# Optimization experiments

Measured on AMD Instinct MI355X. Metric: run time of the kernel, lower is better.

The kernel has to match this reference:

```python
import jax, jax.numpy as jnp
import numpy as np

B, NEG = 4, 33          # queries, candidates per query
N, R = 10000, 256       # entities, relation types (even; R//2 direct)
D, L = 64, 6            # hidden dim, conv layers
E, ER = 200000, 80000   # entity edges, edges per relation graph (hh/ht/th/tt)
F = 2 * D
EPS = 1e-5


def _ln(x, s, b):
    m = jnp.mean(x, -1, keepdims=True)
    v = jnp.mean((x - m) ** 2, -1, keepdims=True)
    return (x - m) * jax.lax.rsqrt(v + EPS) * s + b


def _conv(x, boundary, relation, src, dst, etype, p):
    # GeneralizedRelationalConv (dependent=False, project_relations=True):
    # distmult message, sum aggregate + boundary self-loop, update=relu(LN(Linear([x,agg])))
    p1w, p1b, p2w, p2b, lw, lb, lns, lnb = p
    rel = jax.nn.relu(relation @ p1w + p1b) @ p2w + p2b     # relation projection MLP
    msg = x[:, src, :] * rel[:, etype, :]                   # [B, Eg, D] gathered messages
    agg = jnp.zeros_like(boundary).at[:, dst, :].add(msg) + boundary
    out = jnp.concatenate([x, agg], -1) @ lw + lb
    return jax.nn.relu(_ln(out, lns, lnb))


def _entity_bf(rel_reps, h0, r0, src, dst, etype, params):
    # NBFNet Bellman-Ford over the entity graph, query-conditioned boundary
    q = rel_reps[jnp.arange(B), r0]                         # [B, D]
    boundary = jnp.zeros((B, N, D), q.dtype).at[jnp.arange(B), h0].add(q)
    x = boundary
    for i in range(L):
        x = _conv(x, boundary, rel_reps, src, dst, etype,
                  tuple(t[i] for t in params)) + x          # short_cut residual
    nq = jnp.broadcast_to(q[:, None, :], (B, N, D))
    return jnp.concatenate([x, nq], -1)                     # [B, N, 2D]


def _forward(floats, ints):
    (e1p1w, e1p1b, e1p2w, e1p2b, e1lw, e1lb, e1lns, e1lnb,
     e2p1w, e2p1b, e2p2w, e2p2b, e2lw, e2lb, e2lns, e2lnb,
     e2m1w, e2m1b, e2m2w, e2m2b,
     rp1w, rp1b, rp2w, rp2b, rlw, rlb, rlns, rlnb, nmw, nmb) = floats
    edge_src, edge_dst, edge_type, rel_src, rel_dst, rel_etype, batch = ints
    h0 = batch[:, 0, 0]
    t_idx = batch[:, :, 1]
    r0 = batch[:, 0, 2]
    e1p = (e1p1w, e1p1b, e1p2w, e1p2b, e1lw, e1lb, e1lns, e1lnb)
    # ---- RelNet over the 4 relation graphs (nodes=relations, edge types=entities) ----
    node_reps = jnp.ones((B, N, D), e1p1w.dtype)
    q = jnp.ones((B, D), e1p1w.dtype)
    boundary = jnp.zeros((B, R, D), q.dtype).at[jnp.arange(B), r0].add(q)
    x = boundary
    for i in range(L):
        h = sum(_conv(x, boundary, node_reps, rel_src[g], rel_dst[g], rel_etype[g],
                      (rp1w[g, i], rp1b[g, i], rp2w[g, i], rp2b[g, i],
                       rlw[g, i], rlb[g, i], rlns[g, i], rlnb[g, i]))
                for g in range(4))
        x = h + x                                           # short_cut
        if i == 0:
            # entity_model_1 refreshes the per-entity (relation-graph edge type) reps
            feat = _entity_bf(x, h0, r0, edge_src, edge_dst, edge_type, e1p)
            node_reps = feat @ nmw + nmb                    # [B, N, D]
    rel_reps = x                                            # [B, R, D]
    # ---- EntityNet 2: score candidates ----
    e2p = (e2p1w, e2p1b, e2p2w, e2p2b, e2lw, e2lb, e2lns, e2lnb)
    feat2 = _entity_bf(rel_reps, h0, r0, edge_src, edge_dst, edge_type, e2p)
    g = jnp.take_along_axis(feat2, jnp.broadcast_to(t_idx[:, :, None], (B, NEG, F)), axis=1)
    score = (jax.nn.relu(g @ e2m1w + e2m1b) @ e2m2w + e2m2b)[..., 0]
    return score                                            # [B, NEG]


def setup_inputs():
    key = jax.random.key(0)
    ks = iter(jax.random.split(key, 64))
    def w(shape, std=0.08):
        return jax.random.normal(next(ks), shape, jnp.float32) * std
    inp = {}
    inp["edge_src"] = jax.random.randint(next(ks), (E,), 0, N, jnp.int32)
    inp["edge_dst"] = jax.random.randint(next(ks), (E,), 0, N, jnp.int32)
    inp["edge_type"] = jax.random.randint(next(ks), (E,), 0, R, jnp.int32)
    inp["rel_src"] = jax.random.randint(next(ks), (4, ER), 0, R, jnp.int32)
    inp["rel_dst"] = jax.random.randint(next(ks), (4, ER), 0, R, jnp.int32)
    inp["rel_etype"] = jax.random.randint(next(ks), (4, ER), 0, N, jnp.int32)
    h = jax.random.randint(next(ks), (B, 1), 0, N, jnp.int32)
    t = jax.random.randint(next(ks), (B, NEG), 0, N, jnp.int32)
    r = jax.random.randint(next(ks), (B, 1), 0, R // 2, jnp.int32)
    inp["batch"] = jnp.stack([jnp.broadcast_to(h, (B, NEG)), t,
                              jnp.broadcast_to(r, (B, NEG))], -1)
    for pre in ("e1", "e2"):
        inp[pre + "p1w"] = w((L, D, D)); inp[pre + "p1b"] = jnp.zeros((L, D))
        inp[pre + "p2w"] = w((L, D, D)); inp[pre + "p2b"] = jnp.zeros((L, D))
        inp[pre + "lw"] = w((L, F, D));  inp[pre + "lb"] = jnp.zeros((L, D))
        inp[pre + "lns"] = jnp.ones((L, D)); inp[pre + "lnb"] = jnp.zeros((L, D))
    inp["e2m1w"] = w((F, F)); inp["e2m1b"] = jnp.zeros((F,))
    inp["e2m2w"] = w((F, 1)); inp["e2m2b"] = jnp.zeros((1,))
    inp["rp1w"] = w((4, L, D, D)); inp["rp1b"] = jnp.zeros((4, L, D))
    inp["rp2w"] = w((4, L, D, D)); inp["rp2b"] = jnp.zeros((4, L, D))
    inp["rlw"] = w((4, L, F, D));  inp["rlb"] = jnp.zeros((4, L, D))
    inp["rlns"] = jnp.ones((4, L, D)); inp["rlnb"] = jnp.zeros((4, L, D))
    inp["nmw"] = w((F, D)); inp["nmb"] = jnp.zeros((D,))
    return inp


def reference(e1p1w, e1p1b, e1p2w, e1p2b, e1lw, e1lb, e1lns, e1lnb,
              e2p1w, e2p1b, e2p2w, e2p2b, e2lw, e2lb, e2lns, e2lnb,
              e2m1w, e2m1b, e2m2w, e2m2b,
              rp1w, rp1b, rp2w, rp2b, rlw, rlb, rlns, rlnb, nmw, nmb,
              edge_src, edge_dst, edge_type, rel_src, rel_dst, rel_etype, batch):
    floats = (e1p1w, e1p1b, e1p2w, e1p2b, e1lw, e1lb, e1lns, e1lnb,
              e2p1w, e2p1b, e2p2w, e2p2b, e2lw, e2lb, e2lns, e2lnb,
              e2m1w, e2m1b, e2m2w, e2m2b,
              rp1w, rp1b, rp2w, rp2b, rlw, rlb, rlns, rlnb, nmw, nmb)
    ints = (edge_src, edge_dst, edge_type, rel_src, rel_dst, rel_etype, batch)
    return _forward(floats, ints)
```

## Files before the change

### kernel.cpp

```cpp
#include <hip/hip_runtime.h>

constexpr int kB   = 4;
constexpr int kNEG = 33;
constexpr int kN   = 10000;
constexpr int kR   = 256;
constexpr int kD   = 64;
constexpr int kL   = 6;
constexpr int kE   = 200000;
constexpr int kER  = 80000;

typedef const float* fp;
typedef __attribute__((ext_vector_type(8))) short bf16x8;
typedef __attribute__((ext_vector_type(4))) float f32x4;

__device__ __forceinline__ float rdlane(float v, int l) {
  return __uint_as_float(__builtin_amdgcn_readlane(__float_as_uint(v), l));
}
__device__ __forceinline__ float wave_sum64(float v) {
  #pragma unroll
  for (int o = 32; o > 0; o >>= 1) v += __shfl_xor(v, o, 64);
  return v;
}
__device__ __forceinline__ float group_sum16(float v) {
  #pragma unroll
  for (int o = 8; o > 0; o >>= 1) v += __shfl_xor(v, o, 64);
  return v;
}
__device__ __forceinline__ short f2bf(float x) {
  unsigned u = __float_as_uint(x);
  unsigned r = (u + 0x7fffu + ((u >> 16) & 1u)) >> 16;
  return (short)r;
}
__device__ __forceinline__ float bf2f_u(unsigned short s) {
  return __uint_as_float(((unsigned)s) << 16);
}
__device__ __forceinline__ float bf2f(short s) { return bf2f_u((unsigned short)s); }

__global__ void k_fill(float* __restrict__ p, float v, int n) {
  int i = blockIdx.x * blockDim.x + threadIdx.x;
  int stride = gridDim.x * blockDim.x;
  for (; i < n; i += stride) p[i] = v;
}
__global__ void k_zero_i(int* __restrict__ p, int n) {
  int i = blockIdx.x * blockDim.x + threadIdx.x;
  int stride = gridDim.x * blockDim.x;
  for (; i < n; i += stride) p[i] = 0;
}
__global__ void k_add_row(float* __restrict__ dst, const int* __restrict__ batch) {
  int tid = threadIdx.x;
  int b = tid >> 6, d = tid & 63;
  int row = batch[b * kNEG * 3 + 2];
  dst[((size_t)b * kR + row) * 64 + d] += 1.0f;
}
__global__ void k_add_row_ent(float* __restrict__ dst, const int* __restrict__ batch,
                              const float* __restrict__ q) {
  int tid = threadIdx.x;
  int b = tid >> 6, d = tid & 63;
  int row = batch[b * kNEG * 3];
  dst[((size_t)b * kN + row) * 64 + d] += q[b * 64 + d];
}
__global__ void k_get_q(float* __restrict__ q, const float* __restrict__ relx,
                        const int* __restrict__ batch) {
  int tid = threadIdx.x;
  int b = tid >> 6, d = tid & 63;
  int r0 = batch[b * kNEG * 3 + 2];
  q[b * 64 + d] = relx[((size_t)b * kR + r0) * 64 + d];
}

__global__ void k_hist(const int* __restrict__ dst, int ne, int* __restrict__ cnt) {
  int i = blockIdx.x * blockDim.x + threadIdx.x;
  if (i < ne) atomicAdd(&cnt[dst[i]], 1);
}
__global__ void k_fill_csr(const int* __restrict__ src, const int* __restrict__ dst,
                           const int* __restrict__ et, int ne,
                           int* __restrict__ cursor, int2* __restrict__ out) {
  int i = blockIdx.x * blockDim.x + threadIdx.x;
  if (i < ne) {
    int p = atomicAdd(&cursor[dst[i]], 1);
    out[p] = make_int2(src[i], et[i]);
  }
}
__global__ void k_hist_rel_lds(const int* __restrict__ rel_dst, int* __restrict__ cnt) {
  int g = blockIdx.y;
  __shared__ int lc[256];
  lc[threadIdx.x] = 0;
  __syncthreads();
  int lo = blockIdx.x * 8000, hi = min(lo + 8000, kER);
  for (int e = lo + threadIdx.x; e < hi; e += 256)
    atomicAdd(&lc[rel_dst[(size_t)g * kER + e]], 1);
  __syncthreads();
  int c = lc[threadIdx.x];
  if (c) atomicAdd(&cnt[g * 256 + threadIdx.x], c);
}
__global__ void k_fill_rel_lds(const int* __restrict__ src, const int* __restrict__ dst,
                               const int* __restrict__ et,
                               int* __restrict__ cursor, int2* __restrict__ out) {
  int g = blockIdx.y;
  __shared__ int lc[256];
  lc[threadIdx.x] = 0;
  __syncthreads();
  int lo = blockIdx.x * 8000, hi = min(lo + 8000, kER);
  const int* db = dst + (size_t)g * kER;
  for (int e = lo + threadIdx.x; e < hi; e += 256)
    atomicAdd(&lc[db[e]], 1);
  __syncthreads();
  int c = lc[threadIdx.x];
  __syncthreads();
  lc[threadIdx.x] = c ? atomicAdd(&cursor[g * 257 + threadIdx.x], c) : 0;
  __syncthreads();
  for (int e = lo + threadIdx.x; e < hi; e += 256) {
    int bin = db[e];
    int p = atomicAdd(&lc[bin], 1);
    out[(size_t)g * kER + p] = make_int2(src[(size_t)g * kER + e], et[(size_t)g * kER + e]);
  }
}
__global__ void k_scan_multi(const int* __restrict__ cnt, int* __restrict__ start,
                             int* __restrict__ cursor, int n, int cstride, int sstride) {
  const int* c = cnt + (size_t)blockIdx.x * cstride;
  int* st = start + (size_t)blockIdx.x * sstride;
  int* cu = cursor + (size_t)blockIdx.x * sstride;
  __shared__ int part[256];
  int t = threadIdx.x;
  int chunk = (n + 255) / 256;
  int lo = t * chunk, hi = min(lo + chunk, n);
  int s = 0;
  for (int i = lo; i < hi; ++i) s += c[i];
  part[t] = s;
  __syncthreads();
  if (t == 0) { int run = 0; for (int i = 0; i < 256; ++i) { int v = part[i]; part[i] = run; run += v; } }
  __syncthreads();
  int run = part[t];
  for (int i = lo; i < hi; ++i) { st[i] = run; cu[i] = run; run += c[i]; }
  if (t == 255) st[n] = run;
}

__global__ void k_packw(const float* __restrict__ w1, const float* __restrict__ w2,
                        short* __restrict__ w1h, short* __restrict__ w1l,
                        short* __restrict__ w2h, short* __restrict__ w2l) {
  int pg = blockIdx.x;
  for (int i = threadIdx.x; i < 4096; i += 256) {
    int t = i & 7, lane = (i >> 3) & 63, nt = (i >> 9) & 3, ks = i >> 11;
    int mr = lane & 15, kg = lane >> 4;
    int src = pg * 4096 + (ks * 32 + kg * 8 + t) * 64 + nt * 16 + mr;
    int dst = pg * 4096 + i;
    float v1 = w1[src]; short h1 = f2bf(v1);
    w1h[dst] = h1; w1l[dst] = f2bf(v1 - bf2f(h1));
    float v2 = w2[src]; short h2 = f2bf(v2);
    w2h[dst] = h2; w2l[dst] = f2bf(v2 - bf2f(h2));
  }
}
__global__ void k_packw_e(const float* __restrict__ w, short* __restrict__ wh, short* __restrict__ wl) {
  int set = blockIdx.x;
  for (int i = threadIdx.x; i < 8192; i += 256) {
    int t = i & 7, lane = (i >> 3) & 63, nt = (i >> 9) & 3, ks = i >> 11;
    int mr = lane & 15, kg = lane >> 4;
    int src = set * 8192 + (ks * 32 + kg * 8 + t) * 64 + nt * 16 + mr;
    int dst = set * 8192 + i;
    float v = w[src]; short h = f2bf(v);
    wh[dst] = h; wl[dst] = f2bf(v - bf2f(h));
  }
}

__global__ void __launch_bounds__(256) k_mlp_mfma(
    const float* __restrict__ in, const short* __restrict__ w1h, const short* __restrict__ w1l,
    const float* __restrict__ b1, const short* __restrict__ w2h, const short* __restrict__ w2l,
    const float* __restrict__ b2, int layer, unsigned short* __restrict__ out) {
  int g = blockIdx.y;
  int pg = g * kL + layer;
  int w = threadIdx.x >> 6, lane = threadIdx.x & 63;
  int mrow = lane & 15, kgrp = lane >> 4;
  int r0 = blockIdx.x * 64 + w * 16;
  __shared__ float hbuf[4][16][68];
  const float* xp = in + (size_t)(r0 + mrow) * 64 + kgrp * 8;
  bf16x8 a1h[2], a1l[2];
  #pragma unroll
  for (int ks = 0; ks < 2; ++ks) {
    #pragma unroll
    for (int t = 0; t < 8; ++t) {
      float v = xp[ks * 32 + t];
      short h = f2bf(v); a1h[ks][t] = h; a1l[ks][t] = f2bf(v - bf2f(h));
    }
  }
  const bf16x8* B1h = (const bf16x8*)(w1h + (size_t)pg * 4096);
  const bf16x8* B1l = (const bf16x8*)(w1l + (size_t)pg * 4096);
  #pragma unroll
  for (int nt = 0; nt < 4; ++nt) {
    f32x4 c = {0.f, 0.f, 0.f, 0.f};
    #pragma unroll
    for (int ks = 0; ks < 2; ++ks) {
      bf16x8 bh = B1h[(ks * 4 + nt) * 64 + lane];
      bf16x8 bl = B1l[(ks * 4 + nt) * 64 + lane];
      c = __builtin_amdgcn_mfma_f32_16x16x32_bf16(a1h[ks], bh, c, 0, 0, 0);
      c = __builtin_amdgcn_mfma_f32_16x16x32_bf16(a1h[ks], bl, c, 0, 0, 0);
      c = __builtin_amdgcn_mfma_f32_16x16x32_bf16(a1l[ks], bh, c, 0, 0, 0);
    }
    int col = nt * 16 + mrow;
    float bv = b1[pg * 64 + col];
    #pragma unroll
    for (int rg = 0; rg < 4; ++rg)
      hbuf[w][kgrp * 4 + rg][col] = fmaxf(c[rg] + bv, 0.f);
  }
  __syncthreads();
  bf16x8 a2h[2], a2l[2];
  #pragma unroll
  for (int ks = 0; ks < 2; ++ks) {
    #pragma unroll
    for (int t = 0; t < 8; ++t) {
      float v = hbuf[w][mrow][ks * 32 + kgrp * 8 + t];
      short h = f2bf(v); a2h[ks][t] = h; a2l[ks][t] = f2bf(v - bf2f(h));
    }
  }
  const bf16x8* B2h = (const bf16x8*)(w2h + (size_t)pg * 4096);
  const bf16x8* B2l = (const bf16x8*)(w2l + (size_t)pg * 4096);
  unsigned short* ob = out + (size_t)g * kB * kN * 64;
  #pragma unroll
  for (int nt = 0; nt < 4; ++nt) {
    f32x4 c = {0.f, 0.f, 0.f, 0.f};
    #pragma unroll
    for (int ks = 0; ks < 2; ++ks) {
      bf16x8 bh = B2h[(ks * 4 + nt) * 64 + lane];
      bf16x8 bl = B2l[(ks * 4 + nt) * 64 + lane];
      c = __builtin_amdgcn_mfma_f32_16x16x32_bf16(a2h[ks], bh, c, 0, 0, 0);
      c = __builtin_amdgcn_mfma_f32_16x16x32_bf16(a2h[ks], bl, c, 0, 0, 0);
      c = __builtin_amdgcn_mfma_f32_16x16x32_bf16(a2l[ks], bh, c, 0, 0, 0);
    }
    int col = nt * 16 + mrow;
    float bv = b2[pg * 64 + col];
    #pragma unroll
    for (int rg = 0; rg < 4; ++rg) {
      int grow = r0 + kgrp * 4 + rg;
      int bb = grow / kN;
      int nn = grow - bb * kN;
      ob[(size_t)nn * 256 + col * 4 + bb] = (unsigned short)f2bf(c[rg] + bv);
    }
  }
}

__global__ void __launch_bounds__(256) k_mlp_rel6(
    const float* __restrict__ in, fp p1w, fp p1b, fp p2w, fp p2b,
    unsigned short* __restrict__ out) {
  int j = blockIdx.y;
  int row = blockIdx.x * 4 + (threadIdx.x >> 6);
  int lane = threadIdx.x & 63;
  fp W1 = p1w + (size_t)j * 4096;
  fp W2 = p2w + (size_t)j * 4096;
  float xv = in[(size_t)row * 64 + lane];
  float a = p1b[j * 64 + lane];
  float wbuf[8];
  #pragma unroll
  for (int kk = 0; kk < 64; kk += 8) {
    #pragma unroll
    for (int u = 0; u < 8; ++u) wbuf[u] = W1[(kk + u) * 64 + lane];
    #pragma unroll
    for (int u = 0; u < 8; ++u) a = fmaf(rdlane(xv, kk + u), wbuf[u], a);
  }
  a = fmaxf(a, 0.f);
  float c = p2b[j * 64 + lane];
  #pragma unroll
  for (int kk = 0; kk < 64; kk += 8) {
    #pragma unroll
    for (int u = 0; u < 8; ++u) wbuf[u] = W2[(kk + u) * 64 + lane];
    #pragma unroll
    for (int u = 0; u < 8; ++u) c = fmaf(rdlane(a, kk + u), wbuf[u], c);
  }
  int b = row >> 8, r = row & 255;
  out[((size_t)j * kR + r) * 256 + lane * 4 + b] = (unsigned short)f2bf(c);
}

__global__ void k_gate0(fp p1w, fp p1b, fp p2w, fp p2b, float* __restrict__ gate0) {
  int g = threadIdx.x >> 6, lane = threadIdx.x & 63;
  int pg = g * kL;
  float a = p1b[pg * 64 + lane];
  #pragma unroll
  for (int k = 0; k < 64; ++k) a += p1w[(size_t)pg * 4096 + k * 64 + lane];
  a = fmaxf(a, 0.f);
  float c = p2b[pg * 64 + lane];
  #pragma unroll
  for (int k = 0; k < 64; ++k)
    c = fmaf(rdlane(a, k), p2w[(size_t)pg * 4096 + k * 64 + lane], c);
  gate0[g * 64 + lane] = c;
}
__global__ void k_rel_agg0(const int* __restrict__ rel_start, const int2* __restrict__ rel_edges,
                           const int* __restrict__ batch, const float* __restrict__ gate0,
                           float* __restrict__ agg) {
  int wid = (blockIdx.x * blockDim.x + threadIdx.x) >> 6;
  int lane = threadIdx.x & 63;
  int g = wid >> 10, rem = wid & 1023, b = rem >> 8, r = rem & 255;
  int r0 = batch[b * kNEG * 3 + 2];
  const int* start = rel_start + g * 257;
  const int2* edges = rel_edges + (size_t)g * kER;
  int s0 = start[r], s1 = start[r + 1];
  int cnt = 0;
  for (int base = s0; base < s1; base += 64) {
    int e = base + lane;
    bool m = false;
    if (e < s1) m = (edges[e].x == r0);
    cnt += (int)__popcll(__ballot(m));
  }
  agg[(size_t)wid * 64 + lane] = gate0[g * 64 + lane] * (float)cnt + ((r == r0) ? 1.f : 0.f);
}

__global__ void __launch_bounds__(256) k_gather_rel_all(
    const float* __restrict__ rxi, const unsigned short* __restrict__ gateN,
    const int* __restrict__ rel_start, const int2* __restrict__ rel_edges,
    const int* __restrict__ batch, float* __restrict__ agg) {
  int i = blockIdx.x;
  int g = i & 3, r = i >> 2;
  const unsigned short* gate = gateN + (size_t)g * kB * kN * 64;
  const int* start = rel_start + g * 257;
  const int2* edges = rel_edges + (size_t)g * kER;
  int w = threadIdx.x >> 6, lane = threadIdx.x & 63;
  int s0 = start[r], s1 = start[r + 1];
  int len = s1 - s0;
  int per = (len + 3) >> 2;
  int e0 = s0 + w * per, e1 = min(e0 + per, s1);
  float a0 = 0.f, a1 = 0.f, a2 = 0.f, a3 = 0.f;
  int2 se;
  if (e0 < e1) se = edges[e0];
  for (int e = e0; e < e1; ++e) {
    int2 cur = se;
    if (e + 1 < e1) se = edges[e + 1];
    float4 xv4 = *((const float4*)(rxi + (size_t)cur.x * 256) + lane);
    ushort4 gv4 = *((const ushort4*)(gate + (size_t)cur.y * 256) + lane);
    a0 = fmaf(xv4.x, bf2f_u(gv4.x), a0);
    a1 = fmaf(xv4.y, bf2f_u(gv4.y), a1);
    a2 = fmaf(xv4.z, bf2f_u(gv4.z), a2);
    a3 = fmaf(xv4.w, bf2f_u(gv4.w), a3);
  }
  __shared__ float red[4][4][64];
  red[w][0][lane] = a0; red[w][1][lane] = a1; red[w][2][lane] = a2; red[w][3][lane] = a3;
  __syncthreads();
  float a = red[0][w][lane] + red[1][w][lane] + red[2][w][lane] + red[3][w][lane];
  int r0b = batch[w * kNEG * 3 + 2];
  if (r == r0b) a += 1.0f;
  agg[(((size_t)g * kB + w) * kR + r) * 64 + lane] = a;
}

__global__ void __launch_bounds__(256) k_conv_rel3(
    const float* __restrict__ rel_x, float* __restrict__ agg,
    fp rlw, fp rlb, fp rlns, fp rlnb, int layer) {
  int g = blockIdx.y;
  int pg = g * kL + layer;
  int wave = threadIdx.x >> 6, lane = threadIdx.x & 63;
  int row0 = blockIdx.x * 16 + wave * 4;
  const float* xp = rel_x + (size_t)row0 * 64 + lane;
  float* ap = agg + ((size_t)g * 1024 + row0) * 64 + lane;
  float x0 = xp[0], x1 = xp[64], x2 = xp[128], x3 = xp[192];
  float g0 = ap[0], g1 = ap[64], g2 = ap[128], g3 = ap[192];
  fp w1 = rlw + (size_t)pg * 8192;
  float bv = rlb[pg * 64 + lane];
  float o0 = bv, o1 = bv, o2 = bv, o3 = bv;
  float wbuf[8];
  #pragma unroll
  for (int kk = 0; kk < 128; kk += 8) {
    #pragma unroll
    for (int u = 0; u < 8; ++u) wbuf[u] = w1[(kk + u) * 64 + lane];
    #pragma unroll
    for (int u = 0; u < 8; ++u) {
      int k = kk + u; float w = wbuf[u];
      if (k < 64) {
        o0 = fmaf(rdlane(x0, k), w, o0); o1 = fmaf(rdlane(x1, k), w, o1);
        o2 = fmaf(rdlane(x2, k), w, o2); o3 = fmaf(rdlane(x3, k), w, o3);
      } else {
        o0 = fmaf(rdlane(g0, k - 64), w, o0); o1 = fmaf(rdlane(g1, k - 64), w, o1);
        o2 = fmaf(rdlane(g2, k - 64), w, o2); o3 = fmaf(rdlane(g3, k - 64), w, o3);
      }
    }
  }
  float s = rlns[pg * 64 + lane], t = rlnb[pg * 64 + lane];
  { float m = wave_sum64(o0) * (1.f/64.f); float c = o0 - m;
    float v = wave_sum64(c*c) * (1.f/64.f);
    ap[0] = fmaxf(c * rsqrtf(v + 1e-5f) * s + t, 0.f); }
  { float m = wave_sum64(o1) * (1.f/64.f); float c = o1 - m;
    float v = wave_sum64(c*c) * (1.f/64.f);
    ap[64] = fmaxf(c * rsqrtf(v + 1e-5f) * s + t, 0.f); }
  { float m = wave_sum64(o2) * (1.f/64.f); float c = o2 - m;
    float v = wave_sum64(c*c) * (1.f/64.f);
    ap[128] = fmaxf(c * rsqrtf(v + 1e-5f) * s + t, 0.f); }
  { float m = wave_sum64(o3) * (1.f/64.f); float c = o3 - m;
    float v = wave_sum64(c*c) * (1.f/64.f);
    ap[192] = fmaxf(c * rsqrtf(v + 1e-5f) * s + t, 0.f); }
}

__global__ void k_sum_rel(float* __restrict__ rel_x, float* __restrict__ rxi,
                          const float* __restrict__ y) {
  int i = blockIdx.x * blockDim.x + threadIdx.x;
  float v = rel_x[i] + y[i] + y[65536 + i] + y[131072 + i] + y[196608 + i];
  rel_x[i] = v;
  int d = i & 63, row = i >> 6;
  int b = row >> 8, r = row & 255;
  rxi[(size_t)r * 256 + d * 4 + b] = v;
}

template<bool FIRST>
__global__ void __launch_bounds__(256) k_ent_gather(
    const unsigned short* __restrict__ xbf_cur, const unsigned short* __restrict__ gateL,
    const int* __restrict__ start, const int2* __restrict__ edges,
    const float* __restrict__ q, const int* __restrict__ batch,
    float* __restrict__ agg) {
  int n = (blockIdx.x * blockDim.x + threadIdx.x) >> 6;
  if (n >= kN) return;
  int lane = threadIdx.x & 63;
  int h0[4]; float qv[4];
  #pragma unroll
  for (int b = 0; b < 4; ++b) { h0[b] = batch[b * kNEG * 3]; qv[b] = q[b * 64 + lane]; }
  float a0 = 0.f, a1 = 0.f, a2 = 0.f, a3 = 0.f;
  int s0 = start[n], s1 = start[n + 1];
  int2 se;
  if (s0 < s1) se = edges[s0];
  for (int e = s0; e < s1; ++e) {
    int2 cur = se;
    if (e + 1 < s1) se = edges[e + 1];
    ushort4 gv4 = *((const ushort4*)(gateL + (size_t)cur.y * 256) + lane);
    if (FIRST) {
      if (cur.x == h0[0]) a0 = fmaf(qv[0], bf2f_u(gv4.x), a0);
      if (cur.x == h0[1]) a1 = fmaf(qv[1], bf2f_u(gv4.y), a1);
      if (cur.x == h0[2]) a2 = fmaf(qv[2], bf2f_u(gv4.z), a2);
      if (cur.x == h0[3]) a3 = fmaf(qv[3], bf2f_u(gv4.w), a3);
    } else {
      ushort4 xv4 = *((const ushort4*)(xbf_cur + (size_t)cur.x * 256) + lane);
      a0 = fmaf(bf2f_u(xv4.x), bf2f_u(gv4.x), a0);
      a1 = fmaf(bf2f_u(xv4.y), bf2f_u(gv4.y), a1);
      a2 = fmaf(bf2f_u(xv4.z), bf2f_u(gv4.z), a2);
      a3 = fmaf(bf2f_u(xv4.w), bf2f_u(gv4.w), a3);
    }
  }
  if (n == h0[0]) a0 += qv[0];
  if (n == h0[1]) a1 += qv[1];
  if (n == h0[2]) a2 += qv[2];
  if (n == h0[3]) a3 += qv[3];
  float* ap = agg + (size_t)n * 64 + lane;
  ap[0] = a0; ap[640000] = a1; ap[1280000] = a2; ap[1920000] = a3;
}

__global__ void __launch_bounds__(256) k_ent_conv_mfma(
    const float* __restrict__ xcur, const float* __restrict__ aggv,
    float* __restrict__ xnext, unsigned short* __restrict__ xbf_next,
    const short* __restrict__ wh, const short* __restrict__ wl, int set,
    fp lb, fp lns, fp lnb) {
  int w = threadIdx.x >> 6, lane = threadIdx.x & 63;
  int mrow = lane & 15, kgrp = lane >> 4;
  int r0 = blockIdx.x * 64 + w * 16;
  int arow = r0 + mrow;
  bf16x8 ah[4], al[4];
  #pragma unroll
  for (int ks = 0; ks < 4; ++ks) {
    const float* p = (ks < 2) ? (xcur + (size_t)arow * 64 + ks * 32 + kgrp * 8)
                              : (aggv + (size_t)arow * 64 + (ks - 2) * 32 + kgrp * 8);
    #pragma unroll
    for (int t = 0; t < 8; ++t) {
      float v = p[t];
      short h = f2bf(v); ah[ks][t] = h; al[ks][t] = f2bf(v - bf2f(h));
    }
  }
  const bf16x8* Bh = (const bf16x8*)(wh + (size_t)set * 8192);
  const bf16x8* Bl = (const bf16x8*)(wl + (size_t)set * 8192);
  float o[4][4];
  #pragma unroll
  for (int nt = 0; nt < 4; ++nt) {
    f32x4 c = {0.f, 0.f, 0.f, 0.f};
    #pragma unroll
    for (int ks = 0; ks < 4; ++ks) {
      bf16x8 bh = Bh[(ks * 4 + nt) * 64 + lane];
      bf16x8 bl = Bl[(ks * 4 + nt) * 64 + lane];
      c = __builtin_amdgcn_mfma_f32_16x16x32_bf16(ah[ks], bh, c, 0, 0, 0);
      c = __builtin_amdgcn_mfma_f32_16x16x32_bf16(ah[ks], bl, c, 0, 0, 0);
      c = __builtin_amdgcn_mfma_f32_16x16x32_bf16(al[ks], bh, c, 0, 0, 0);
    }
    float bv = lb[nt * 16 + mrow];
    #pragma unroll
    for (int rg = 0; rg < 4; ++rg) o[nt][rg] = c[rg] + bv;
  }
  float mean[4], varr[4];
  #pragma unroll
  for (int rg = 0; rg < 4; ++rg) {
    float p = o[0][rg] + o[1][rg] + o[2][rg] + o[3][rg];
    mean[rg] = group_sum16(p) * (1.f / 64.f);
    float d0 = o[0][rg] - mean[rg], d1 = o[1][rg] - mean[rg];
    float d2 = o[2][rg] - mean[rg], d3 = o[3][rg] - mean[rg];
    float vs = d0 * d0 + d1 * d1 + d2 * d2 + d3 * d3;
    varr[rg] = group_sum16(vs) * (1.f / 64.f);
  }
  #pragma unroll
  for (int nt = 0; nt < 4; ++nt) {
    int col = nt * 16 + mrow;
    float s = lns[col], tt = lnb[col];
    #pragma unroll
    for (int rg = 0; rg < 4; ++rg) {
      int grow = r0 + kgrp * 4 + rg;
      float xv = xcur[(size_t)grow * 64 + col];
      float y = xv + fmaxf((o[nt][rg] - mean[rg]) * rsqrtf(varr[rg] + 1e-5f) * s + tt, 0.f);
      xnext[(size_t)grow * 64 + col] = y;
      int bb = grow / kN;
      int nn = grow - bb * kN;
      xbf_next[(size_t)nn * 256 + col * 4 + bb] = (unsigned short)f2bf(y);
    }
  }
}

__global__ void __launch_bounds__(256) k_nodeup4(
    const float* __restrict__ x, const float* __restrict__ q,
    fp nmw, fp nmb, float* __restrict__ out) {
  int wid = (blockIdx.x * blockDim.x + threadIdx.x) >> 6;
  int lane = threadIdx.x & 63;
  int r0 = wid * 4;
  if (r0 >= kB * kN) return;
  int b = r0 / kN;
  const float* ip = x + (size_t)r0 * 64 + lane;
  float x0 = ip[0], x1 = ip[64], x2 = ip[128], x3 = ip[192];
  float qv = q[b * 64 + lane];
  float bv = nmb[lane];
  float c0 = bv, c1 = bv, c2 = bv, c3 = bv;
  float wbuf[4];
  #pragma unroll
  for (int kk = 0; kk < 64; kk += 4) {
    #pragma unroll
    for (int u = 0; u < 4; ++u) wbuf[u] = nmw[(kk + u) * 64 + lane];
    #pragma unroll
    for (int u = 0; u < 4; ++u) {
      int k = kk + u; float w = wbuf[u];
      c0 = fmaf(rdlane(x0, k), w, c0); c1 = fmaf(rdlane(x1, k), w, c1);
      c2 = fmaf(rdlane(x2, k), w, c2); c3 = fmaf(rdlane(x3, k), w, c3);
    }
  }
  float qa = 0.f;
  #pragma unroll
  for (int k = 0; k < 64; ++k)
    qa = fmaf(rdlane(qv, k), nmw[(64 + k) * 64 + lane], qa);
  float* op = out + (size_t)r0 * 64 + lane;
  op[0] = c0 + qa; op[64] = c1 + qa; op[128] = c2 + qa; op[192] = c3 + qa;
}

__global__ void k_score(const float* __restrict__ entx, const float* __restrict__ q,
                        const int* __restrict__ batch,
                        fp m1w, fp m1b, fp m2w, fp m2b,
                        float* __restrict__ out) {
  int b = blockIdx.x / kNEG, n = blockIdx.x % kNEG;
  int t = batch[(b * kNEG + n) * 3 + 1];
  int j = threadIdx.x;
  __shared__ float gv[128];
  __shared__ float red[2];
  gv[j] = (j < 64) ? entx[((size_t)b * kN + t) * 64 + j] : q[b * 64 + (j - 64)];
  __syncthreads();
  float acc = m1b[j];
  #pragma unroll 16
  for (int k = 0; k < 128; ++k)
    acc = fmaf(gv[k], m1w[k * 128 + j], acc);
  float h = fmaxf(acc, 0.f) * m2w[j];
  h = wave_sum64(h);
  if ((j & 63) == 0) red[j >> 6] = h;
  __syncthreads();
  if (j == 0) out[b * kNEG + n] = red[0] + red[1] + m2b[0];
}

extern "C" void kernel_launch(void* const* d_in, const int* in_sizes, int n_in,
                              void* d_out, int out_size, void* d_ws, size_t ws_size,
                              hipStream_t stream) {
  const int* edge_src  = (const int*)d_in[0];
  const int* edge_dst  = (const int*)d_in[1];
  const int* edge_type = (const int*)d_in[2];
  const int* rel_src   = (const int*)d_in[3];
  const int* rel_dst   = (const int*)d_in[4];
  const int* rel_etype = (const int*)d_in[5];
  const int* batch     = (const int*)d_in[6];
  fp e1p1w = (fp)d_in[7],  e1p1b = (fp)d_in[8],  e1p2w = (fp)d_in[9],  e1p2b = (fp)d_in[10];
  fp e1lw  = (fp)d_in[11], e1lb  = (fp)d_in[12], e1lns = (fp)d_in[13], e1lnb = (fp)d_in[14];
  fp e2p1w = (fp)d_in[15], e2p1b = (fp)d_in[16], e2p2w = (fp)d_in[17], e2p2b = (fp)d_in[18];
  fp e2lw  = (fp)d_in[19], e2lb  = (fp)d_in[20], e2lns = (fp)d_in[21], e2lnb = (fp)d_in[22];
  fp e2m1w = (fp)d_in[23], e2m1b = (fp)d_in[24], e2m2w = (fp)d_in[25], e2m2b = (fp)d_in[26];
  fp rp1w  = (fp)d_in[27], rp1b  = (fp)d_in[28], rp2w  = (fp)d_in[29], rp2b  = (fp)d_in[30];
  fp rlw   = (fp)d_in[31], rlb   = (fp)d_in[32], rlns  = (fp)d_in[33], rlnb  = (fp)d_in[34];
  fp nmw   = (fp)d_in[35], nmb   = (fp)d_in[36];

  float* ws = (float*)d_ws;
  float* rel_x     = ws;
  float* q         = rel_x + 65536;
  float* gate0     = q + 256;
  float* rxi       = gate0 + 256;
  float* rel_agg   = rxi + 65536;
  float* node_reps = rel_agg + 262144;
  float* ent_xa    = node_reps + 2560000;
  float* ent_xb    = ent_xa + 2560000;
  float* ent_agg   = ent_xb + 2560000;
  unsigned short* gateR6 = (unsigned short*)(ent_agg + 2560000);
  unsigned short* gateN  = gateR6 + 393216;
  unsigned short* ent_ba = gateN + 10240000;
  unsigned short* ent_bb = ent_ba + 2560000;
  int*   iws       = (int*)(ent_bb + 2560000);
  int2*  ent_edges = (int2*)iws;
  int2*  rel_edges = (int2*)(iws + 400000);
  int*   ent_cnt   = iws + 400000 + 640000;
  int*   ent_start = ent_cnt + 10000;
  int*   ent_cur   = ent_start + 10001;
  int*   rel_cnt   = ent_cur + 10001;
  int*   rel_start = rel_cnt + 1024;
  int*   rel_cur   = rel_start + 1028;
  short* w1hp      = (short*)(rel_cur + 1028 + 2);
  short* w1lp      = w1hp + 98304;
  short* w2hp      = w1lp + 98304;
  short* w2lp      = w2hp + 98304;
  short* elwh      = w2lp + 98304;
  short* elwl      = elwh + 98304;

  const int nZero = 10000 + 10001 + 10001 + 1024;
  k_zero_i<<<(nZero + 255) / 256, 256, 0, stream>>>(ent_cnt, nZero);
  k_hist<<<(kE + 255) / 256, 256, 0, stream>>>(edge_dst, kE, ent_cnt);
  k_hist_rel_lds<<<dim3(10, 4), 256, 0, stream>>>(rel_dst, rel_cnt);
  k_scan_multi<<<1, 256, 0, stream>>>(ent_cnt, ent_start, ent_cur, 10000, 0, 0);
  k_scan_multi<<<4, 256, 0, stream>>>(rel_cnt, rel_start, rel_cur, 256, 256, 257);
  k_fill_csr<<<(kE + 255) / 256, 256, 0, stream>>>(edge_src, edge_dst, edge_type, kE, ent_cur, ent_edges);
  k_fill_rel_lds<<<dim3(10, 4), 256, 0, stream>>>(rel_src, rel_dst, rel_etype, rel_cur, rel_edges);
  k_packw<<<24, 256, 0, stream>>>(rp1w, rp2w, w1hp, w1lp, w2hp, w2lp);
  k_packw_e<<<6, 256, 0, stream>>>(e1lw, elwh, elwl);
  k_packw_e<<<6, 256, 0, stream>>>(e2lw, elwh + 6 * 8192, elwl + 6 * 8192);

  k_fill<<<256, 256, 0, stream>>>(rel_x, 0.f, kB * kR * kD);
  k_add_row<<<1, 256, 0, stream>>>(rel_x, batch);

  k_gate0<<<1, 256, 0, stream>>>(rp1w, rp1b, rp2w, rp2b, gate0);
  k_rel_agg0<<<1024, 256, 0, stream>>>(rel_start, rel_edges, batch, gate0, rel_agg);
  k_conv_rel3<<<dim3(64, 4), 256, 0, stream>>>(rel_x, rel_agg, rlw, rlb, rlns, rlnb, 0);
  k_sum_rel<<<256, 256, 0, stream>>>(rel_x, rxi, rel_agg);

  k_get_q<<<1, 256, 0, stream>>>(q, rel_x, batch);
  k_mlp_rel6<<<dim3(256, 6), 256, 0, stream>>>(rel_x, e1p1w, e1p1b, e1p2w, e1p2b, gateR6);
  k_fill<<<2048, 256, 0, stream>>>(ent_xa, 0.f, kB * kN * kD);
  k_add_row_ent<<<1, 256, 0, stream>>>(ent_xa, batch, q);
  {
    float* cur = ent_xa; float* nxt = ent_xb;
    unsigned short* bcur = ent_ba; unsigned short* bnxt = ent_bb;
    for (int j = 0; j < kL; ++j) {
      const unsigned short* gL = gateR6 + (size_t)j * kR * 256;
      if (j == 0)
        k_ent_gather<true><<<2500, 256, 0, stream>>>(bcur, gL, ent_start, ent_edges, q, batch, ent_agg);
      else
        k_ent_gather<false><<<2500, 256, 0, stream>>>(bcur, gL, ent_start, ent_edges, q, batch, ent_agg);
      k_ent_conv_mfma<<<625, 256, 0, stream>>>(cur, ent_agg, nxt, bnxt, elwh, elwl, j,
          e1lb + (size_t)j * 64, e1lns + (size_t)j * 64, e1lnb + (size_t)j * 64);
      float* tf = cur; cur = nxt; nxt = tf;
      unsigned short* tb = bcur; bcur = bnxt; bnxt = tb;
    }
    k_nodeup4<<<2500, 256, 0, stream>>>(cur, q, nmw, nmb, node_reps);
  }

  for (int i = 1; i < kL; ++i) {
    k_mlp_mfma<<<dim3(625, 4), 256, 0, stream>>>(node_reps, w1hp, w1lp, rp1b, w2hp, w2lp, rp2b, i, gateN);
    k_gather_rel_all<<<1024, 256, 0, stream>>>(rxi, gateN, rel_start, rel_edges, batch, rel_agg);
    k_conv_rel3<<<dim3(64, 4), 256, 0, stream>>>(rel_x, rel_agg, rlw, rlb, rlns, rlnb, i);
    k_sum_rel<<<256, 256, 0, stream>>>(rel_x, rxi, rel_agg);
  }

  k_get_q<<<1, 256, 0, stream>>>(q, rel_x, batch);
  k_mlp_rel6<<<dim3(256, 6), 256, 0, stream>>>(rel_x, e2p1w, e2p1b, e2p2w, e2p2b, gateR6);
  k_fill<<<2048, 256, 0, stream>>>(ent_xa, 0.f, kB * kN * kD);
  k_add_row_ent<<<1, 256, 0, stream>>>(ent_xa, batch, q);
  {
    float* cur = ent_xa; float* nxt = ent_xb;
    unsigned short* bcur = ent_ba; unsigned short* bnxt = ent_bb;
    for (int j = 0; j < kL; ++j) {
      const unsigned short* gL = gateR6 + (size_t)j * kR * 256;
      if (j == 0)
        k_ent_gather<true><<<2500, 256, 0, stream>>>(bcur, gL, ent_start, ent_edges, q, batch, ent_agg);
      else
        k_ent_gather<false><<<2500, 256, 0, stream>>>(bcur, gL, ent_start, ent_edges, q, batch, ent_agg);
      k_ent_conv_mfma<<<625, 256, 0, stream>>>(cur, ent_agg, nxt, bnxt, elwh, elwl, 6 + j,
          e2lb + (size_t)j * 64, e2lns + (size_t)j * 64, e2lnb + (size_t)j * 64);
      float* tf = cur; cur = nxt; nxt = tf;
      unsigned short* tb = bcur; bcur = bnxt; bnxt = tb;
    }
    k_score<<<kB * kNEG, 128, 0, stream>>>(cur, q, batch, e2m1w, e2m1b, e2m2w, e2m2b, (float*)d_out);
  }
}
```

Measured before the change: 1.002 ms.

## Switch gathers from batch-interleaved bf16 layout to per-batch fp32 layout

Replaces the node-major, batch-interleaved (n,d,b) layouts used by the entity and relation gathers with batch-major [b][n][d] layouts. Entity gathers now read fp32 state and fp32 gate tensors directly, with one wave per (batch, node), so the bf16 shadow copies of the entity state and the rxi transposed copy are no longer written. The aim is to drop those extra writes and the strided scatter stores. In exchange each edge is now read once per batch instead of once for all four, giving four times the edge-index traffic and narrower per-lane loads, and fp32 gathers double the bytes compared with bf16.

```diff
diff --git a/kernel.cpp b/kernel.cpp
--- a/kernel.cpp
+++ b/kernel.cpp
@@ -229,16 +229,14 @@
     #pragma unroll
     for (int rg = 0; rg < 4; ++rg) {
       int grow = r0 + kgrp * 4 + rg;
-      int bb = grow / kN;
-      int nn = grow - bb * kN;
-      ob[(size_t)nn * 256 + col * 4 + bb] = (unsigned short)f2bf(c[rg] + bv);
+      ob[(size_t)grow * 64 + col] = (unsigned short)f2bf(c[rg] + bv);
     }
   }
 }
 
 __global__ void __launch_bounds__(256) k_mlp_rel6(
     const float* __restrict__ in, fp p1w, fp p1b, fp p2w, fp p2b,
-    unsigned short* __restrict__ out) {
+    float* __restrict__ out) {
   int j = blockIdx.y;
   int row = blockIdx.x * 4 + (threadIdx.x >> 6);
   int lane = threadIdx.x & 63;
@@ -263,8 +261,7 @@
     #pragma unroll
     for (int u = 0; u < 8; ++u) c = fmaf(rdlane(a, kk + u), wbuf[u], c);
   }
-  int b = row >> 8, r = row & 255;
-  out[((size_t)j * kR + r) * 256 + lane * 4 + b] = (unsigned short)f2bf(c);
+  out[((size_t)j * kB * kR + row) * 64 + lane] = c;
 }
 
 __global__ void k_gate0(fp p1w, fp p1b, fp p2w, fp p2b, float* __restrict__ gate0) {
@@ -300,13 +297,15 @@
   agg[(size_t)wid * 64 + lane] = gate0[g * 64 + lane] * (float)cnt + ((r == r0) ? 1.f : 0.f);
 }
 
-__global__ void __launch_bounds__(256) k_gather_rel_all(
-    const float* __restrict__ rxi, const unsigned short* __restrict__ gateN,
+__global__ void __launch_bounds__(256) k_gather_rel_b(
+    const float* __restrict__ rel_x, const unsigned short* __restrict__ gateN,
     const int* __restrict__ rel_start, const int2* __restrict__ rel_edges,
     const int* __restrict__ batch, float* __restrict__ agg) {
   int i = blockIdx.x;
-  int g = i & 3, r = i >> 2;
-  const unsigned short* gate = gateN + (size_t)g * kB * kN * 64;
+  int s = i & 15, r = i >> 4;
+  int g = s >> 2, b = s & 3;
+  const unsigned short* gate = gateN + ((size_t)(g * kB + b) * kN) * 64;
+  const float* xb = rel_x + (size_t)b * kR * 64;
   const int* start = rel_start + g * 257;
   const int2* edges = rel_edges + (size_t)g * kER;
   int w = threadIdx.x >> 6, lane = threadIdx.x & 63;
@@ -314,26 +313,23 @@
   int len = s1 - s0;
   int per = (len + 3) >> 2;
   int e0 = s0 + w * per, e1 = min(e0 + per, s1);
-  float a0 = 0.f, a1 = 0.f, a2 = 0.f, a3 = 0.f;
+  float acc = 0.f;
   int2 se;
   if (e0 < e1) se = edges[e0];
   for (int e = e0; e < e1; ++e) {
     int2 cur = se;
     if (e + 1 < e1) se = edges[e + 1];
-    float4 xv4 = *((const float4*)(rxi + (size_t)cur.x * 256) + lane);
-    ushort4 gv4 = *((const ushort4*)(gate + (size_t)cur.y * 256) + lane);
-    a0 = fmaf(xv4.x, bf2f_u(gv4.x), a0);
-    a1 = fmaf(xv4.y, bf2f_u(gv4.y), a1);
-    a2 = fmaf(xv4.z, bf2f_u(gv4.z), a2);
-    a3 = fmaf(xv4.w, bf2f_u(gv4.w), a3);
-  }
-  __shared__ float red[4][4][64];
-  red[w][0][lane] = a0; red[w][1][lane] = a1; red[w][2][lane] = a2; red[w][3][lane] = a3;
-  __syncthreads();
-  float a = red[0][w][lane] + red[1][w][lane] + red[2][w][lane] + red[3][w][lane];
-  int r0b = batch[w * kNEG * 3 + 2];
-  if (r == r0b) a += 1.0f;
-  agg[(((size_t)g * kB + w) * kR + r) * 64 + lane] = a;
+    acc = fmaf(xb[(size_t)cur.x * 64 + lane], bf2f_u(gate[(size_t)cur.y * 64 + lane]), acc);
+  }
+  __shared__ float red[4][64];
+  red[w][lane] = acc;
+  __syncthreads();
+  if (w == 0) {
+    float a = red[0][lane] + red[1][lane] + red[2][lane] + red[3][lane];
+    int r0b = batch[b * kNEG * 3 + 2];
+    if (r == r0b) a += 1.0f;
+    agg[(((size_t)g * kB + b) * kR + r) * 64 + lane] = a;
+  }
 }
 
 __global__ void __launch_bounds__(256) k_conv_rel3(
@@ -382,60 +378,47 @@
     ap[192] = fmaxf(c * rsqrtf(v + 1e-5f) * s + t, 0.f); }
 }
 
-__global__ void k_sum_rel(float* __restrict__ rel_x, float* __restrict__ rxi,
-                          const float* __restrict__ y) {
+__global__ void k_sum_rel(float* __restrict__ rel_x, const float* __restrict__ y) {
   int i = blockIdx.x * blockDim.x + threadIdx.x;
-  float v = rel_x[i] + y[i] + y[65536 + i] + y[131072 + i] + y[196608 + i];
-  rel_x[i] = v;
-  int d = i & 63, row = i >> 6;
-  int b = row >> 8, r = row & 255;
-  rxi[(size_t)r * 256 + d * 4 + b] = v;
+  rel_x[i] += y[i] + y[65536 + i] + y[131072 + i] + y[196608 + i];
 }
 
 template<bool FIRST>
-__global__ void __launch_bounds__(256) k_ent_gather(
-    const unsigned short* __restrict__ xbf_cur, const unsigned short* __restrict__ gateL,
+__global__ void __launch_bounds__(256) k_ent_gather_b(
+    const float* __restrict__ xcur, const float* __restrict__ gateL,
     const int* __restrict__ start, const int2* __restrict__ edges,
     const float* __restrict__ q, const int* __restrict__ batch,
     float* __restrict__ agg) {
-  int n = (blockIdx.x * blockDim.x + threadIdx.x) >> 6;
-  if (n >= kN) return;
-  int lane = threadIdx.x & 63;
-  int h0[4]; float qv[4];
-  #pragma unroll
-  for (int b = 0; b < 4; ++b) { h0[b] = batch[b * kNEG * 3]; qv[b] = q[b * 64 + lane]; }
-  float a0 = 0.f, a1 = 0.f, a2 = 0.f, a3 = 0.f;
+  int i = blockIdx.x;
+  int rr = i & 7, m = i >> 3;
+  int b = rr >> 1, p = rr & 1;
+  int w = threadIdx.x >> 6, lane = threadIdx.x & 63;
+  int n = ((m * 2 + p) << 2) + w;
+  int h0 = batch[b * kNEG * 3];
+  float qv = q[b * 64 + lane];
+  const float* xb = xcur + (size_t)b * kN * 64;
+  const float* gb = gateL + (size_t)b * kR * 64;
+  float a = 0.f;
   int s0 = start[n], s1 = start[n + 1];
   int2 se;
   if (s0 < s1) se = edges[s0];
   for (int e = s0; e < s1; ++e) {
     int2 cur = se;
     if (e + 1 < s1) se = edges[e + 1];
-    ushort4 gv4 = *((const ushort4*)(gateL + (size_t)cur.y * 256) + lane);
+    float gv = gb[(size_t)cur.y * 64 + lane];
     if (FIRST) {
-      if (cur.x == h0[0]) a0 = fmaf(qv[0], bf2f_u(gv4.x), a0);
-      if (cur.x == h0[1]) a1 = fmaf(qv[1], bf2f_u(gv4.y), a1);
-      if (cur.x == h0[2]) a2 = fmaf(qv[2], bf2f_u(gv4.z), a2);
-      if (cur.x == h0[3]) a3 = fmaf(qv[3], bf2f_u(gv4.w), a3);
+      if (cur.x == h0) a = fmaf(qv, gv, a);
     } else {
-      ushort4 xv4 = *((const ushort4*)(xbf_cur + (size_t)cur.x * 256) + lane);
-      a0 = fmaf(bf2f_u(xv4.x), bf2f_u(gv4.x), a0);
-      a1 = fmaf(bf2f_u(xv4.y), bf2f_u(gv4.y), a1);
-      a2 = fmaf(bf2f_u(xv4.z), bf2f_u(gv4.z), a2);
-      a3 = fmaf(bf2f_u(xv4.w), bf2f_u(gv4.w), a3);
-    }
-  }
-  if (n == h0[0]) a0 += qv[0];
-  if (n == h0[1]) a1 += qv[1];
-  if (n == h0[2]) a2 += qv[2];
-  if (n == h0[3]) a3 += qv[3];
-  float* ap = agg + (size_t)n * 64 + lane;
-  ap[0] = a0; ap[640000] = a1; ap[1280000] = a2; ap[1920000] = a3;
+      a = fmaf(xb[(size_t)cur.x * 64 + lane], gv, a);
+    }
+  }
+  if (n == h0) a += qv;
+  agg[(size_t)b * kN * 64 + (size_t)n * 64 + lane] = a;
 }
 
 __global__ void __launch_bounds__(256) k_ent_conv_mfma(
     const float* __restrict__ xcur, const float* __restrict__ aggv,
-    float* __restrict__ xnext, unsigned short* __restrict__ xbf_next,
+    float* __restrict__ xnext,
     const short* __restrict__ wh, const short* __restrict__ wl, int set,
     fp lb, fp lns, fp lnb) {
   int w = threadIdx.x >> 6, lane = threadIdx.x & 63;
@@ -491,9 +474,6 @@
       float xv = xcur[(size_t)grow * 64 + col];
       float y = xv + fmaxf((o[nt][rg] - mean[rg]) * rsqrtf(varr[rg] + 1e-5f) * s + tt, 0.f);
       xnext[(size_t)grow * 64 + col] = y;
-      int bb = grow / kN;
-      int nn = grow - bb * kN;
-      xbf_next[(size_t)nn * 256 + col * 4 + bb] = (unsigned short)f2bf(y);
     }
   }
 }
@@ -576,17 +556,14 @@
   float* rel_x     = ws;
   float* q         = rel_x + 65536;
   float* gate0     = q + 256;
-  float* rxi       = gate0 + 256;
-  float* rel_agg   = rxi + 65536;
+  float* gateR6f   = gate0 + 256;
+  float* rel_agg   = gateR6f + 393216;
   float* node_reps = rel_agg + 262144;
   float* ent_xa    = node_reps + 2560000;
   float* ent_xb    = ent_xa + 2560000;
   float* ent_agg   = ent_xb + 2560000;
-  unsigned short* gateR6 = (unsigned short*)(ent_agg + 2560000);
-  unsigned short* gateN  = gateR6 + 393216;
-  unsigned short* ent_ba = gateN + 10240000;
-  unsigned short* ent_bb = ent_ba + 2560000;
-  int*   iws       = (int*)(ent_bb + 2560000);
+  unsigned short* gateN = (unsigned short*)(ent_agg + 2560000);
+  int*   iws       = (int*)(gateN + 10240000);
   int2*  ent_edges = (int2*)iws;
   int2*  rel_edges = (int2*)(iws + 400000);
   int*   ent_cnt   = iws + 400000 + 640000;
@@ -620,53 +597,49 @@
   k_gate0<<<1, 256, 0, stream>>>(rp1w, rp1b, rp2w, rp2b, gate0);
   k_rel_agg0<<<1024, 256, 0, stream>>>(rel_start, rel_edges, batch, gate0, rel_agg);
   k_conv_rel3<<<dim3(64, 4), 256, 0, stream>>>(rel_x, rel_agg, rlw, rlb, rlns, rlnb, 0);
-  k_sum_rel<<<256, 256, 0, stream>>>(rel_x, rxi, rel_agg);
+  k_sum_rel<<<256, 256, 0, stream>>>(rel_x, rel_agg);
 
   k_get_q<<<1, 256, 0, stream>>>(q, rel_x, batch);
-  k_mlp_rel6<<<dim3(256, 6), 256, 0, stream>>>(rel_x, e1p1w, e1p1b, e1p2w, e1p2b, gateR6);
+  k_mlp_rel6<<<dim3(256, 6), 256, 0, stream>>>(rel_x, e1p1w, e1p1b, e1p2w, e1p2b, gateR6f);
   k_fill<<<2048, 256, 0, stream>>>(ent_xa, 0.f, kB * kN * kD);
   k_add_row_ent<<<1, 256, 0, stream>>>(ent_xa, batch, q);
   {
     float* cur = ent_xa; float* nxt = ent_xb;
-    unsigned short* bcur = ent_ba; unsigned short* bnxt = ent_bb;
     for (int j = 0; j < kL; ++j) {
-      const unsigned short* gL = gateR6 + (size_t)j * kR * 256;
+      const float* gL = gateR6f + (size_t)j * kB * kR * 64;
       if (j == 0)
-        k_ent_gather<true><<<2500, 256, 0, stream>>>(bcur, gL, ent_start, ent_edges, q, batch, ent_agg);
+        k_ent_gather_b<true><<<10000, 256, 0, stream>>>(cur, gL, ent_start, ent_edges, q, batch, ent_agg);
       else
-        k_ent_gather<false><<<2500, 256, 0, stream>>>(bcur, gL, ent_start, ent_edges, q, batch, ent_agg);
-      k_ent_conv_mfma<<<625, 256, 0, stream>>>(cur, ent_agg, nxt, bnxt, elwh, elwl, j,
+        k_ent_gather_b<false><<<10000, 256, 0, stream>>>(cur, gL, ent_start, ent_edges, q, batch, ent_agg);
+      k_ent_conv_mfma<<<625, 256, 0, stream>>>(cur, ent_agg, nxt, elwh, elwl, j,
           e1lb + (size_t)j * 64, e1lns + (size_t)j * 64, e1lnb + (size_t)j * 64);
       float* tf = cur; cur = nxt; nxt = tf;
-      unsigned short* tb = bcur; bcur = bnxt; bnxt = tb;
     }
     k_nodeup4<<<2500, 256, 0, stream>>>(cur, q, nmw, nmb, node_reps);
   }
 
   for (int i = 1; i < kL; ++i) {
     k_mlp_mfma<<<dim3(625, 4), 256, 0, stream>>>(node_reps, w1hp, w1lp, rp1b, w2hp, w2lp, rp2b, i, gateN);
-    k_gather_rel_all<<<1024, 256, 0, stream>>>(rxi, gateN, rel_start, rel_edges, batch, rel_agg);
+    k_gather_rel_b<<<4096, 256, 0, stream>>>(rel_x, gateN, rel_start, rel_edges, batch, rel_agg);
     k_conv_rel3<<<dim3(64, 4), 256, 0, stream>>>(rel_x, rel_agg, rlw, rlb, rlns, rlnb, i);
-    k_sum_rel<<<256, 256, 0, stream>>>(rel_x, rxi, rel_agg);
+    k_sum_rel<<<256, 256, 0, stream>>>(rel_x, rel_agg);
   }
 
   k_get_q<<<1, 256, 0, stream>>>(q, rel_x, batch);
-  k_mlp_rel6<<<dim3(256, 6), 256, 0, stream>>>(rel_x, e2p1w, e2p1b, e2p2w, e2p2b, gateR6);
+  k_mlp_rel6<<<dim3(256, 6), 256, 0, stream>>>(rel_x, e2p1w, e2p1b, e2p2w, e2p2b, gateR6f);
   k_fill<<<2048, 256, 0, stream>>>(ent_xa, 0.f, kB * kN * kD);
   k_add_row_ent<<<1, 256, 0, stream>>>(ent_xa, batch, q);
   {
     float* cur = ent_xa; float* nxt = ent_xb;
-    unsigned short* bcur = ent_ba; unsigned short* bnxt = ent_bb;
     for (int j = 0; j < kL; ++j) {
-      const unsigned short* gL = gateR6 + (size_t)j * kR * 256;
+      const float* gL = gateR6f + (size_t)j * kB * kR * 64;
       if (j == 0)
-        k_ent_gather<true><<<2500, 256, 0, stream>>>(bcur, gL, ent_start, ent_edges, q, batch, ent_agg);
+        k_ent_gather_b<true><<<10000, 256, 0, stream>>>(cur, gL, ent_start, ent_edges, q, batch, ent_agg);
       else
-        k_ent_gather<false><<<2500, 256, 0, stream>>>(bcur, gL, ent_start, ent_edges, q, batch, ent_agg);
-      k_ent_conv_mfma<<<625, 256, 0, stream>>>(cur, ent_agg, nxt, bnxt, elwh, elwl, 6 + j,
+        k_ent_gather_b<false><<<10000, 256, 0, stream>>>(cur, gL, ent_start, ent_edges, q, batch, ent_agg);
+      k_ent_conv_mfma<<<625, 256, 0, stream>>>(cur, ent_agg, nxt, elwh, elwl, 6 + j,
           e2lb + (size_t)j * 64, e2lns + (size_t)j * 64, e2lnb + (size_t)j * 64);
       float* tf = cur; cur = nxt; nxt = tf;
-      unsigned short* tb = bcur; bcur = bnxt; bnxt = tb;
     }
     k_score<<<kB * kNEG, 128, 0, stream>>>(cur, q, batch, e2m1w, e2m1b, e2m2w, e2m2b, (float*)d_out);
   }
```

After: 1.294 ms. 29.1% more time.
